# Optimization experiments

Measured on AMD Instinct MI355X. Metric: run time of the kernel, lower is better.

Reference implementation:

```python
import jax, jax.numpy as jnp
import numpy as np

HIDDEN = 512
IN_FEAT = 512


def setup_inputs() -> dict:
    key = jax.random.key(0)
    ks = jax.random.split(key, 6)
    x = jax.random.normal(ks[0], (128, 1024, IN_FEAT), dtype=jnp.float32)
    # LSTM params: concatenated gates in flax order (i, f, g, o)
    s_in = 1.0 / np.sqrt(IN_FEAT)
    s_h = 1.0 / np.sqrt(HIDDEN)
    Wi = jax.random.normal(ks[1], (IN_FEAT, 4 * HIDDEN), dtype=jnp.float32) * s_in
    Wh = jax.random.normal(ks[2], (HIDDEN, 4 * HIDDEN), dtype=jnp.float32) * s_h
    b = jnp.zeros((4 * HIDDEN,), dtype=jnp.float32)
    Wd = jax.random.normal(ks[3], (HIDDEN, 1), dtype=jnp.float32) * s_h
    bd = jnp.zeros((1,), dtype=jnp.float32)
    return {"x": x, "Wi": Wi, "Wh": Wh, "b": b, "Wd": Wd, "bd": bd}


def reference(x, Wi, Wh, b, Wd, bd):
    B, S, _ = x.shape
    H = Wh.shape[0]
    c0 = jnp.zeros((B, H), dtype=x.dtype)
    h0 = jnp.zeros((B, H), dtype=x.dtype)

    def step(carry, xt):
        c, h = carry
        gates = xt @ Wi + h @ Wh + b  # [B, 4H]
        i, f, g, o = jnp.split(gates, 4, axis=-1)
        c_new = jax.nn.sigmoid(f) * c + jax.nn.sigmoid(i) * jnp.tanh(g)
        h_new = jax.nn.sigmoid(o) * jnp.tanh(c_new)
        return (c_new, h_new), None

    (c_T, h_T), _ = jax.lax.scan(step, (c0, h0), jnp.swapaxes(x, 0, 1))
    # Dense(1) on last timestep output, then squeeze
    return (h_T @ Wd + bd).squeeze(-1)
```

## Files before the change

### kernel.cpp

```cpp
#include <hip/hip_runtime.h>

typedef unsigned int u32;
typedef unsigned short u16;
typedef unsigned long long u64;
typedef float f32x4 __attribute__((ext_vector_type(4)));
typedef _Float16 f16x8 __attribute__((ext_vector_type(8)));

#define S_LEN 1024
#define NG 8
#define NM 32
#define GBAT 16
#define PSTR 20

__device__ __forceinline__ u16 f2h_bits(float f) {
  _Float16 h = (_Float16)f;
  return __builtin_bit_cast(u16, h);
}
__device__ __forceinline__ float h2f_bits(u16 b) {
  return (float)__builtin_bit_cast(_Float16, b);
}
__device__ __forceinline__ u32 pk2(float a, float b) {
  return (u32)f2h_bits(a) | ((u32)f2h_bits(b) << 16);
}
__device__ __forceinline__ u32 pkh(u64 v) {
  return (u32)(v & 0xFFFFu) | (((u32)(v >> 32) & 0xFFFFu) << 16);
}

__global__ __launch_bounds__(256) void prep_frags(const float* __restrict__ Wi,
                                                  const float* __restrict__ Wh,
                                                  uint4* __restrict__ wf4) {
  const int blk = blockIdx.x;
  const int m = blk & 31;
  const float* __restrict__ W = (blk & 32) ? Wh : Wi;
  uint4* __restrict__ dst = wf4 + ((blk & 32) ? 131072 : 0) + m * 4096;
  for (int fi = threadIdx.x; fi < 4096; fi += 256) {
    const int lane = fi & 63;
    const int kc = (fi >> 6) & 15;
    const int q = fi >> 10;
    const int gq = lane >> 4, c = lane & 15;
    const int kb = kc * 32 + gq * 8;
    const int gcol = q * 512 + m * 16 + c;
    u32 wds[4];
#pragma unroll
    for (int pp = 0; pp < 4; ++pp) {
      u16 e0 = f2h_bits(W[(size_t)(kb + 2 * pp) * 2048 + gcol]);
      u16 e1 = f2h_bits(W[(size_t)(kb + 2 * pp + 1) * 2048 + gcol]);
      wds[pp] = (u32)e0 | ((u32)e1 << 16);
    }
    uint4 v; v.x = wds[0]; v.y = wds[1]; v.z = wds[2]; v.w = wds[3];
    dst[fi] = v;
  }
}

__global__ __launch_bounds__(256) void lstm_main(
    const float* __restrict__ x,
    const uint4* __restrict__ wif4,
    u32* __restrict__ hbuf,
    const float* __restrict__ bvec,
    const float* __restrict__ Wd,
    const float* __restrict__ bd,
    float* __restrict__ out) {
  __shared__ __align__(16) uint4 sWi[4096];
  __shared__ __align__(16) uint4 sWh[4096];
  __shared__ __align__(16) float pred[16][PSTR * 16];

  const int tid = threadIdx.x;
  const int lane = tid & 63;
  const int wv = tid >> 6;
  const int g = blockIdx.x & 7;
  const int m = blockIdx.x >> 3;

  for (int i = tid; i < 4096; i += 256) {
    sWi[i] = wif4[m * 4096 + i];
    sWh[i] = wif4[131072 + m * 4096 + i];
  }

  const int bt = tid >> 4;
  const int hi_ = tid & 15;
  const int gb = g * GBAT + bt;
  const int hidx = m * 16 + hi_;

  const float bi = bvec[hidx];
  const float bf_ = bvec[512 + hidx];
  const float bg = bvec[1024 + hidx];
  const float bo = bvec[1536 + hidx];
  float c_reg = 0.f;

  const int abt = lane & 15;
  const int oct = lane >> 4;
  const float* __restrict__ xrow = x + (size_t)(g * GBAT + abt) * (S_LEN * 512);
  const u32 hrow_off = ((u32)(g * GBAT + abt)) << 9;

  __syncthreads();

  float4 xa[8], xb[8];
#pragma unroll
  for (int kk = 0; kk < 4; ++kk) {
    const int k0 = ((wv << 2) | kk) * 32 + oct * 8;
    xa[2 * kk]     = *reinterpret_cast<const float4*>(xrow + k0);
    xa[2 * kk + 1] = *reinterpret_cast<const float4*>(xrow + k0 + 4);
  }

  auto step = [&](int t, float4* cur, float4* nxt) {
    {
      int tn = t + 1; tn = (tn < S_LEN) ? tn : (S_LEN - 1);
      const float* xr = xrow + (size_t)tn * 512;
#pragma unroll
      for (int kk = 0; kk < 4; ++kk) {
        const int k0 = ((wv << 2) | kk) * 32 + oct * 8;
        nxt[2 * kk]     = *reinterpret_cast<const float4*>(xr + k0);
        nxt[2 * kk + 1] = *reinterpret_cast<const float4*>(xr + k0 + 4);
      }
    }

    f32x4 acc0 = {0.f, 0.f, 0.f, 0.f}, acc1 = acc0, acc2 = acc0, acc3 = acc0;
#pragma unroll
    for (int kk = 0; kk < 4; ++kk) {
      const int kc = (wv << 2) | kk;
      uint4 av;
      av.x = pk2(cur[2 * kk].x, cur[2 * kk].y);
      av.y = pk2(cur[2 * kk].z, cur[2 * kk].w);
      av.z = pk2(cur[2 * kk + 1].x, cur[2 * kk + 1].y);
      av.w = pk2(cur[2 * kk + 1].z, cur[2 * kk + 1].w);
      f16x8 af = __builtin_bit_cast(f16x8, av);
      acc0 = __builtin_amdgcn_mfma_f32_16x16x32_f16(af, __builtin_bit_cast(f16x8, sWi[(0 * 16 + kc) * 64 + lane]), acc0, 0, 0, 0);
      acc1 = __builtin_amdgcn_mfma_f32_16x16x32_f16(af, __builtin_bit_cast(f16x8, sWi[(1 * 16 + kc) * 64 + lane]), acc1, 0, 0, 0);
      acc2 = __builtin_amdgcn_mfma_f32_16x16x32_f16(af, __builtin_bit_cast(f16x8, sWi[(2 * 16 + kc) * 64 + lane]), acc2, 0, 0, 0);
      acc3 = __builtin_amdgcn_mfma_f32_16x16x32_f16(af, __builtin_bit_cast(f16x8, sWi[(3 * 16 + kc) * 64 + lane]), acc3, 0, 0, 0);
    }

    if (t > 0) {
      const u64* hp = reinterpret_cast<const u64*>(hbuf + (u32)(t & 1) * 65536u + hrow_off);
      const u32 want = (u32)t;
      const u64 wpat = ((u64)want << 16) | ((u64)want << 48);
      u64 raw[4][4];
      for (;;) {
#pragma unroll
        for (int kk = 0; kk < 4; ++kk) {
          const int base = (((wv << 2) | kk) << 4) | (oct << 2);
#pragma unroll
          for (int ee = 0; ee < 4; ++ee)
            raw[kk][ee] = __hip_atomic_load(hp + base + ee, __ATOMIC_RELAXED,
                                            __HIP_MEMORY_SCOPE_AGENT);
        }
        __builtin_amdgcn_sched_barrier(0);
        u64 chk = 0;
#pragma unroll
        for (int kk = 0; kk < 4; ++kk)
#pragma unroll
          for (int ee = 0; ee < 4; ++ee)
            chk |= (raw[kk][ee] ^ wpat) & 0xFFFF0000FFFF0000ull;
        if (__all(chk == 0)) break;
        __builtin_amdgcn_s_sleep(1);
      }
      uint4 hv[4];
#pragma unroll
      for (int kk = 0; kk < 4; ++kk) {
        uint4 t4;
        t4.x = pkh(raw[kk][0]); t4.y = pkh(raw[kk][1]);
        t4.z = pkh(raw[kk][2]); t4.w = pkh(raw[kk][3]);
        hv[kk] = t4;
      }
#pragma unroll
      for (int kk = 0; kk < 4; ++kk) {
        const int kc = (wv << 2) | kk;
        f16x8 hf = __builtin_bit_cast(f16x8, hv[kk]);
        acc0 = __builtin_amdgcn_mfma_f32_16x16x32_f16(hf, __builtin_bit_cast(f16x8, sWh[(0 * 16 + kc) * 64 + lane]), acc0, 0, 0, 0);
        acc1 = __builtin_amdgcn_mfma_f32_16x16x32_f16(hf, __builtin_bit_cast(f16x8, sWh[(1 * 16 + kc) * 64 + lane]), acc1, 0, 0, 0);
        acc2 = __builtin_amdgcn_mfma_f32_16x16x32_f16(hf, __builtin_bit_cast(f16x8, sWh[(2 * 16 + kc) * 64 + lane]), acc2, 0, 0, 0);
        acc3 = __builtin_amdgcn_mfma_f32_16x16x32_f16(hf, __builtin_bit_cast(f16x8, sWh[(3 * 16 + kc) * 64 + lane]), acc3, 0, 0, 0);
      }
    }

    {
      const int cc = lane & 15;
      const int r0 = (lane >> 4) << 2;
      *reinterpret_cast<f32x4*>(&pred[wv * 4 + 0][PSTR * cc + r0]) = acc0;
      *reinterpret_cast<f32x4*>(&pred[wv * 4 + 1][PSTR * cc + r0]) = acc1;
      *reinterpret_cast<f32x4*>(&pred[wv * 4 + 2][PSTR * cc + r0]) = acc2;
      *reinterpret_cast<f32x4*>(&pred[wv * 4 + 3][PSTR * cc + r0]) = acc3;
    }
    asm volatile("s_waitcnt lgkmcnt(0)" ::: "memory");
    __builtin_amdgcn_s_barrier();
    __builtin_amdgcn_sched_barrier(0);

    {
      float gi = bi, gf = bf_, gg = bg, go = bo;
#pragma unroll
      for (int w2 = 0; w2 < 4; ++w2) {
        gi += pred[w2 * 4 + 0][PSTR * hi_ + bt];
        gf += pred[w2 * 4 + 1][PSTR * hi_ + bt];
        gg += pred[w2 * 4 + 2][PSTR * hi_ + bt];
        go += pred[w2 * 4 + 3][PSTR * hi_ + bt];
      }
      const float si = 1.f / (1.f + __expf(-gi));
      const float sf = 1.f / (1.f + __expf(-gf));
      const float so = 1.f / (1.f + __expf(-go));
      c_reg = sf * c_reg + si * tanhf(gg);
      const float hv_ = so * tanhf(c_reg);
      const u32 word = ((u32)(t + 1) << 16) | (u32)f2h_bits(hv_);
      __hip_atomic_store(hbuf + (u32)((t + 1) & 1) * 65536u + (u32)gb * 512u + (u32)hidx,
                         word, __ATOMIC_RELAXED, __HIP_MEMORY_SCOPE_AGENT);
    }
    __builtin_amdgcn_s_barrier();
    __builtin_amdgcn_sched_barrier(0);
  };

  for (int t = 0; t < S_LEN; t += 2) {
    step(t, xa, xb);
    step(t + 1, xb, xa);
  }

  if (m == 0) {
    const int btf = tid >> 4;
    const int part = tid & 15;
    const u64* hp = reinterpret_cast<const u64*>(hbuf + (((u32)(g * GBAT + btf)) << 9));
    const u32 want = (u32)S_LEN;
    const u64 wpat = ((u64)want << 16) | ((u64)want << 48);
    u64 rawv[16];
    for (;;) {
#pragma unroll
      for (int j2 = 0; j2 < 16; ++j2)
        rawv[j2] = __hip_atomic_load(hp + part * 16 + j2, __ATOMIC_RELAXED,
                                     __HIP_MEMORY_SCOPE_AGENT);
      __builtin_amdgcn_sched_barrier(0);
      u64 chk = 0;
#pragma unroll
      for (int j2 = 0; j2 < 16; ++j2)
        chk |= (rawv[j2] ^ wpat) & 0xFFFF0000FFFF0000ull;
      if (__all(chk == 0)) break;
      __builtin_amdgcn_s_sleep(1);
    }
    float acc = 0.f;
#pragma unroll
    for (int j2 = 0; j2 < 16; ++j2) {
      const int k = part * 32 + 2 * j2;
      acc += h2f_bits((u16)(rawv[j2] & 0xFFFFu)) * Wd[k] +
             h2f_bits((u16)((rawv[j2] >> 32) & 0xFFFFu)) * Wd[k + 1];
    }
#pragma unroll
    for (int s = 1; s < 16; s <<= 1) acc += __shfl_xor(acc, s, 64);
    if (part == 0) out[g * GBAT + btf] = acc + bd[0];
  }
}

extern "C" void kernel_launch(void* const* d_in, const int* in_sizes, int n_in,
                              void* d_out, int out_size, void* d_ws, size_t ws_size,
                              hipStream_t stream) {
  const float* x = (const float*)d_in[0];
  const float* Wi = (const float*)d_in[1];
  const float* Wh = (const float*)d_in[2];
  const float* bv = (const float*)d_in[3];
  const float* Wd = (const float*)d_in[4];
  const float* bd = (const float*)d_in[5];
  float* out = (float*)d_out;

  char* ws = (char*)d_ws;
  uint4* wif4 = (uint4*)ws;
  u32* hbuf = (u32*)(ws + (4u << 20));

  hipLaunchKernelGGL(prep_frags, dim3(64), dim3(256), 0, stream, Wi, Wh, wif4);

  const float* kx = x;
  const uint4* kw = wif4;
  u32* kh = hbuf;
  const float* kbv = bv;
  const float* kwd = Wd;
  const float* kbd = bd;
  float* ko = out;
  void* args[] = {&kx, &kw, &kh, &kbv, &kwd, &kbd, &ko};
  hipLaunchCooperativeKernel(reinterpret_cast<void*>(lstm_main), dim3(NG * NM),
                             dim3(256), args, 0, stream);
}
```

Baseline: 4.217 ms.

## Replace per-element tagged h words with per-block step flags and packed fp16 h

Each h value used to carry its own step tag inside a 32-bit word, and consumers polled every word until all tags matched. Producers now write dense packed fp16 pairs, wait for their stores to drain, then one thread per block publishes a step counter. Consumers spin on 32 flags per batch group and then read h once with half the bytes. The next-step x prefetch is moved after the flag wait. The cost is an extra vmcnt(0) wait plus barrier-then-flag latency on the critical path, and correctness now depends on relaxed-ordering visibility between the data stores and the flag store.

```diff
diff --git a/kernel.cpp b/kernel.cpp
--- a/kernel.cpp
+++ b/kernel.cpp
@@ -22,14 +22,13 @@
 __device__ __forceinline__ u32 pk2(float a, float b) {
   return (u32)f2h_bits(a) | ((u32)f2h_bits(b) << 16);
 }
-__device__ __forceinline__ u32 pkh(u64 v) {
-  return (u32)(v & 0xFFFFu) | (((u32)(v >> 32) & 0xFFFFu) << 16);
-}
 
 __global__ __launch_bounds__(256) void prep_frags(const float* __restrict__ Wi,
                                                   const float* __restrict__ Wh,
-                                                  uint4* __restrict__ wf4) {
+                                                  uint4* __restrict__ wf4,
+                                                  u32* __restrict__ flags) {
   const int blk = blockIdx.x;
+  if (blk == 0) flags[threadIdx.x] = 0;
   const int m = blk & 31;
   const float* __restrict__ W = (blk & 32) ? Wh : Wi;
   uint4* __restrict__ dst = wf4 + ((blk & 32) ? 131072 : 0) + m * 4096;
@@ -55,7 +54,8 @@
 __global__ __launch_bounds__(256) void lstm_main(
     const float* __restrict__ x,
     const uint4* __restrict__ wif4,
-    u32* __restrict__ hbuf,
+    u16* __restrict__ hbuf16,
+    u32* __restrict__ flags,
     const float* __restrict__ bvec,
     const float* __restrict__ Wd,
     const float* __restrict__ bd,
@@ -89,7 +89,10 @@
   const int abt = lane & 15;
   const int oct = lane >> 4;
   const float* __restrict__ xrow = x + (size_t)(g * GBAT + abt) * (S_LEN * 512);
-  const u32 hrow_off = ((u32)(g * GBAT + abt)) << 9;
+  const u32 drow = ((u32)(g * GBAT + abt)) * 128u;
+  u32* const hb32 = reinterpret_cast<u32*>(hbuf16);
+  const u64* const hb64 = reinterpret_cast<const u64*>(hbuf16);
+  u32* const flg = flags + g * 32;
 
   __syncthreads();
 
@@ -102,17 +105,6 @@
   }
 
   auto step = [&](int t, float4* cur, float4* nxt) {
-    {
-      int tn = t + 1; tn = (tn < S_LEN) ? tn : (S_LEN - 1);
-      const float* xr = xrow + (size_t)tn * 512;
-#pragma unroll
-      for (int kk = 0; kk < 4; ++kk) {
-        const int k0 = ((wv << 2) | kk) * 32 + oct * 8;
-        nxt[2 * kk]     = *reinterpret_cast<const float4*>(xr + k0);
-        nxt[2 * kk + 1] = *reinterpret_cast<const float4*>(xr + k0 + 4);
-      }
-    }
-
     f32x4 acc0 = {0.f, 0.f, 0.f, 0.f}, acc1 = acc0, acc2 = acc0, acc3 = acc0;
 #pragma unroll
     for (int kk = 0; kk < 4; ++kk) {
@@ -130,45 +122,55 @@
     }
 
     if (t > 0) {
-      const u64* hp = reinterpret_cast<const u64*>(hbuf + (u32)(t & 1) * 65536u + hrow_off);
       const u32 want = (u32)t;
-      const u64 wpat = ((u64)want << 16) | ((u64)want << 48);
-      u64 raw[4][4];
       for (;;) {
+        u32 fv = __hip_atomic_load(flg + (lane & 31), __ATOMIC_RELAXED,
+                                   __HIP_MEMORY_SCOPE_AGENT);
+        if (__all(fv >= want)) break;
+        __builtin_amdgcn_s_sleep(1);
+      }
+      __builtin_amdgcn_sched_barrier(0);
+      asm volatile("" ::: "memory");
+
+      {
+        int tn = t + 1; tn = (tn < S_LEN) ? tn : (S_LEN - 1);
+        const float* xr = xrow + (size_t)tn * 512;
 #pragma unroll
         for (int kk = 0; kk < 4; ++kk) {
-          const int base = (((wv << 2) | kk) << 4) | (oct << 2);
-#pragma unroll
-          for (int ee = 0; ee < 4; ++ee)
-            raw[kk][ee] = __hip_atomic_load(hp + base + ee, __ATOMIC_RELAXED,
-                                            __HIP_MEMORY_SCOPE_AGENT);
+          const int k0 = ((wv << 2) | kk) * 32 + oct * 8;
+          nxt[2 * kk]     = *reinterpret_cast<const float4*>(xr + k0);
+          nxt[2 * kk + 1] = *reinterpret_cast<const float4*>(xr + k0 + 4);
         }
-        __builtin_amdgcn_sched_barrier(0);
-        u64 chk = 0;
-#pragma unroll
-        for (int kk = 0; kk < 4; ++kk)
-#pragma unroll
-          for (int ee = 0; ee < 4; ++ee)
-            chk |= (raw[kk][ee] ^ wpat) & 0xFFFF0000FFFF0000ull;
-        if (__all(chk == 0)) break;
-        __builtin_amdgcn_s_sleep(1);
-      }
-      uint4 hv[4];
+      }
+
+      const u32 dbase = ((u32)(t & 1)) * 16384u + drow;
+      u64 raw[4][2];
 #pragma unroll
       for (int kk = 0; kk < 4; ++kk) {
-        uint4 t4;
-        t4.x = pkh(raw[kk][0]); t4.y = pkh(raw[kk][1]);
-        t4.z = pkh(raw[kk][2]); t4.w = pkh(raw[kk][3]);
-        hv[kk] = t4;
-      }
+        const u32 ci = dbase + (u32)(((wv << 2) | kk) * 8 + oct * 2);
+        raw[kk][0] = __hip_atomic_load(hb64 + ci, __ATOMIC_RELAXED, __HIP_MEMORY_SCOPE_AGENT);
+        raw[kk][1] = __hip_atomic_load(hb64 + ci + 1, __ATOMIC_RELAXED, __HIP_MEMORY_SCOPE_AGENT);
+      }
+      __builtin_amdgcn_sched_barrier(0);
 #pragma unroll
       for (int kk = 0; kk < 4; ++kk) {
         const int kc = (wv << 2) | kk;
-        f16x8 hf = __builtin_bit_cast(f16x8, hv[kk]);
+        uint4 t4;
+        t4.x = (u32)raw[kk][0]; t4.y = (u32)(raw[kk][0] >> 32);
+        t4.z = (u32)raw[kk][1]; t4.w = (u32)(raw[kk][1] >> 32);
+        f16x8 hf = __builtin_bit_cast(f16x8, t4);
         acc0 = __builtin_amdgcn_mfma_f32_16x16x32_f16(hf, __builtin_bit_cast(f16x8, sWh[(0 * 16 + kc) * 64 + lane]), acc0, 0, 0, 0);
         acc1 = __builtin_amdgcn_mfma_f32_16x16x32_f16(hf, __builtin_bit_cast(f16x8, sWh[(1 * 16 + kc) * 64 + lane]), acc1, 0, 0, 0);
         acc2 = __builtin_amdgcn_mfma_f32_16x16x32_f16(hf, __builtin_bit_cast(f16x8, sWh[(2 * 16 + kc) * 64 + lane]), acc2, 0, 0, 0);
         acc3 = __builtin_amdgcn_mfma_f32_16x16x32_f16(hf, __builtin_bit_cast(f16x8, sWh[(3 * 16 + kc) * 64 + lane]), acc3, 0, 0, 0);
+      }
+    } else {
+      const float* xr = xrow + 512;
+#pragma unroll
+      for (int kk = 0; kk < 4; ++kk) {
+        const int k0 = ((wv << 2) | kk) * 32 + oct * 8;
+        nxt[2 * kk]     = *reinterpret_cast<const float4*>(xr + k0);
+        nxt[2 * kk + 1] = *reinterpret_cast<const float4*>(xr + k0 + 4);
       }
     }
 
@@ -198,12 +200,19 @@
       const float so = 1.f / (1.f + __expf(-go));
       c_reg = sf * c_reg + si * tanhf(gg);
       const float hv_ = so * tanhf(c_reg);
-      const u32 word = ((u32)(t + 1) << 16) | (u32)f2h_bits(hv_);
-      __hip_atomic_store(hbuf + (u32)((t + 1) & 1) * 65536u + (u32)gb * 512u + (u32)hidx,
-                         word, __ATOMIC_RELAXED, __HIP_MEMORY_SCOPE_AGENT);
-    }
+      const u32 hb = (u32)f2h_bits(hv_);
+      const u32 partner = __shfl_xor(hb, 1, 64);
+      if ((hi_ & 1) == 0) {
+        const u32 word = hb | (partner << 16);
+        const u32 wi_ = ((u32)((t + 1) & 1)) * 32768u + (u32)gb * 256u + ((u32)hidx >> 1);
+        __hip_atomic_store(hb32 + wi_, word, __ATOMIC_RELAXED, __HIP_MEMORY_SCOPE_AGENT);
+      }
+    }
+    asm volatile("s_waitcnt vmcnt(0)" ::: "memory");
     __builtin_amdgcn_s_barrier();
     __builtin_amdgcn_sched_barrier(0);
+    if (tid == 0)
+      __hip_atomic_store(flg + m, (u32)(t + 1), __ATOMIC_RELAXED, __HIP_MEMORY_SCOPE_AGENT);
   };
 
   for (int t = 0; t < S_LEN; t += 2) {
@@ -214,29 +223,29 @@
   if (m == 0) {
     const int btf = tid >> 4;
     const int part = tid & 15;
-    const u64* hp = reinterpret_cast<const u64*>(hbuf + (((u32)(g * GBAT + btf)) << 9));
-    const u32 want = (u32)S_LEN;
-    const u64 wpat = ((u64)want << 16) | ((u64)want << 48);
-    u64 rawv[16];
     for (;;) {
-#pragma unroll
-      for (int j2 = 0; j2 < 16; ++j2)
-        rawv[j2] = __hip_atomic_load(hp + part * 16 + j2, __ATOMIC_RELAXED,
-                                     __HIP_MEMORY_SCOPE_AGENT);
-      __builtin_amdgcn_sched_barrier(0);
-      u64 chk = 0;
-#pragma unroll
-      for (int j2 = 0; j2 < 16; ++j2)
-        chk |= (rawv[j2] ^ wpat) & 0xFFFF0000FFFF0000ull;
-      if (__all(chk == 0)) break;
+      u32 fv = __hip_atomic_load(flg + (lane & 31), __ATOMIC_RELAXED,
+                                 __HIP_MEMORY_SCOPE_AGENT);
+      if (__all(fv >= (u32)S_LEN)) break;
       __builtin_amdgcn_s_sleep(1);
     }
+    __builtin_amdgcn_sched_barrier(0);
+    asm volatile("" ::: "memory");
+    const u32 rbase = ((u32)(g * GBAT + btf)) * 128u + (u32)part * 8u;
+    u64 rawv[8];
+#pragma unroll
+    for (int j = 0; j < 8; ++j)
+      rawv[j] = __hip_atomic_load(hb64 + rbase + j, __ATOMIC_RELAXED,
+                                  __HIP_MEMORY_SCOPE_AGENT);
+    __builtin_amdgcn_sched_barrier(0);
     float acc = 0.f;
 #pragma unroll
-    for (int j2 = 0; j2 < 16; ++j2) {
-      const int k = part * 32 + 2 * j2;
-      acc += h2f_bits((u16)(rawv[j2] & 0xFFFFu)) * Wd[k] +
-             h2f_bits((u16)((rawv[j2] >> 32) & 0xFFFFu)) * Wd[k + 1];
+    for (int j = 0; j < 8; ++j) {
+      const int k = part * 32 + 4 * j;
+      acc += h2f_bits((u16)(rawv[j] & 0xFFFFu)) * Wd[k] +
+             h2f_bits((u16)((rawv[j] >> 16) & 0xFFFFu)) * Wd[k + 1] +
+             h2f_bits((u16)((rawv[j] >> 32) & 0xFFFFu)) * Wd[k + 2] +
+             h2f_bits((u16)((rawv[j] >> 48) & 0xFFFFu)) * Wd[k + 3];
     }
 #pragma unroll
     for (int s = 1; s < 16; s <<= 1) acc += __shfl_xor(acc, s, 64);
@@ -257,18 +266,20 @@
 
   char* ws = (char*)d_ws;
   uint4* wif4 = (uint4*)ws;
-  u32* hbuf = (u32*)(ws + (4u << 20));
-
-  hipLaunchKernelGGL(prep_frags, dim3(64), dim3(256), 0, stream, Wi, Wh, wif4);
+  u16* hbuf16 = (u16*)(ws + (4u << 20));
+  u32* flags = (u32*)(ws + (4u << 20) + (256u << 10));
+
+  hipLaunchKernelGGL(prep_frags, dim3(64), dim3(256), 0, stream, Wi, Wh, wif4, flags);
 
   const float* kx = x;
   const uint4* kw = wif4;
-  u32* kh = hbuf;
+  u16* kh = hbuf16;
+  u32* kf = flags;
   const float* kbv = bv;
   const float* kwd = Wd;
   const float* kbd = bd;
   float* ko = out;
-  void* args[] = {&kx, &kw, &kh, &kbv, &kwd, &kbd, &ko};
-  hipLaunchCooperativeKernel(reinterpret_cast<void*>(lstm_main), dim3(NG * NM),
-                             dim3(256), args, 0, stream);
-}
+  void* args[] = {&kx, &kw, &kh, &kf, &kbv, &kwd, &kbd, &ko};
+  (void)hipLaunchCooperativeKernel(reinterpret_cast<void*>(lstm_main), dim3(NG * NM),
+                                   dim3(256), args, 0, stream);
+}
```

After: 4.334 ms. 1.03x slower.

## Add XCC-local fast path for h exchange using sc0 vector loads

Applied to the files above, without the earlier changes.

At startup each block records its XCC id and checks whether all 32 blocks of its batch group sit on the same XCC. If they do, the hidden-state exchange polls a second buffer with wide sc0 (cache-coherent within the XCC) dwordx4 loads instead of device-scope atomic loads, and falls back to the atomic path after a bounded spin count. Each h value is written to both buffers. The next-x prefetch is also moved after the h wait to shorten the critical path. This adds redundant stores and depends on how the hardware places blocks, and a missed cross-XCC visibility case could cost up to 512 spins per step before the fallback takes over.

```diff
diff --git a/kernel.cpp b/kernel.cpp
--- a/kernel.cpp
+++ b/kernel.cpp
@@ -5,6 +5,7 @@
 typedef unsigned long long u64;
 typedef float f32x4 __attribute__((ext_vector_type(4)));
 typedef _Float16 f16x8 __attribute__((ext_vector_type(8)));
+typedef u32 u32x4 __attribute__((ext_vector_type(4)));
 
 #define S_LEN 1024
 #define NG 8
@@ -28,8 +29,10 @@
 
 __global__ __launch_bounds__(256) void prep_frags(const float* __restrict__ Wi,
                                                   const float* __restrict__ Wh,
-                                                  uint4* __restrict__ wf4) {
+                                                  uint4* __restrict__ wf4,
+                                                  u32* __restrict__ det) {
   const int blk = blockIdx.x;
+  if (blk == 0) det[threadIdx.x] = 0;
   const int m = blk & 31;
   const float* __restrict__ W = (blk & 32) ? Wh : Wi;
   uint4* __restrict__ dst = wf4 + ((blk & 32) ? 131072 : 0) + m * 4096;
@@ -56,6 +59,8 @@
     const float* __restrict__ x,
     const uint4* __restrict__ wif4,
     u32* __restrict__ hbuf,
+    u32* __restrict__ hbuf2,
+    u32* __restrict__ det,
     const float* __restrict__ bvec,
     const float* __restrict__ Wd,
     const float* __restrict__ bd,
@@ -93,6 +98,24 @@
 
   __syncthreads();
 
+  bool fastw;
+  {
+    u32 myxcc;
+    asm volatile("s_getreg_b32 %0, hwreg(HW_REG_XCC_ID)" : "=s"(myxcc));
+    if (tid == 0)
+      __hip_atomic_store(det + g * 32 + m, myxcc + 1u, __ATOMIC_RELAXED,
+                         __HIP_MEMORY_SCOPE_AGENT);
+    u32 dv;
+    for (;;) {
+      dv = __hip_atomic_load(det + g * 32 + (lane & 31), __ATOMIC_RELAXED,
+                             __HIP_MEMORY_SCOPE_AGENT);
+      if (__all(dv != 0u)) break;
+      __builtin_amdgcn_s_sleep(1);
+    }
+    const u32 d0 = __shfl(dv, 0, 64);
+    fastw = __all(dv == d0);
+  }
+
   float4 xa[8], xb[8];
 #pragma unroll
   for (int kk = 0; kk < 4; ++kk) {
@@ -102,17 +125,6 @@
   }
 
   auto step = [&](int t, float4* cur, float4* nxt) {
-    {
-      int tn = t + 1; tn = (tn < S_LEN) ? tn : (S_LEN - 1);
-      const float* xr = xrow + (size_t)tn * 512;
-#pragma unroll
-      for (int kk = 0; kk < 4; ++kk) {
-        const int k0 = ((wv << 2) | kk) * 32 + oct * 8;
-        nxt[2 * kk]     = *reinterpret_cast<const float4*>(xr + k0);
-        nxt[2 * kk + 1] = *reinterpret_cast<const float4*>(xr + k0 + 4);
-      }
-    }
-
     f32x4 acc0 = {0.f, 0.f, 0.f, 0.f}, acc1 = acc0, acc2 = acc0, acc3 = acc0;
 #pragma unroll
     for (int kk = 0; kk < 4; ++kk) {
@@ -130,37 +142,91 @@
     }
 
     if (t > 0) {
-      const u64* hp = reinterpret_cast<const u64*>(hbuf + (u32)(t & 1) * 65536u + hrow_off);
-      const u32 want = (u32)t;
-      const u64 wpat = ((u64)want << 16) | ((u64)want << 48);
-      u64 raw[4][4];
-      for (;;) {
+      const u32 tg = (u32)t << 16;
+      uint4 hv[4];
+      bool got = false;
+
+      if (fastw) {
+        const u32* p2 = hbuf2 + (((u32)(t & 1)) << 16) + hrow_off +
+                        ((u32)((wv << 7) | (oct << 3)));
+        int spins = 0;
+        for (;;) {
+          u32x4 fA0, fB0, fA1, fB1, fA2, fB2, fA3, fB3;
+          asm volatile("global_load_dwordx4 %0, %1, off sc0" : "=&v"(fA0) : "v"(p2));
+          asm volatile("global_load_dwordx4 %0, %1, off offset:16 sc0" : "=&v"(fB0) : "v"(p2));
+          asm volatile("global_load_dwordx4 %0, %1, off offset:128 sc0" : "=&v"(fA1) : "v"(p2));
+          asm volatile("global_load_dwordx4 %0, %1, off offset:144 sc0" : "=&v"(fB1) : "v"(p2));
+          asm volatile("global_load_dwordx4 %0, %1, off offset:256 sc0" : "=&v"(fA2) : "v"(p2));
+          asm volatile("global_load_dwordx4 %0, %1, off offset:272 sc0" : "=&v"(fB2) : "v"(p2));
+          asm volatile("global_load_dwordx4 %0, %1, off offset:384 sc0" : "=&v"(fA3) : "v"(p2));
+          asm volatile("global_load_dwordx4 %0, %1, off offset:400 sc0" : "=&v"(fB3) : "v"(p2));
+          asm volatile("s_waitcnt vmcnt(0)" ::: "memory");
+          __builtin_amdgcn_sched_barrier(0);
+          u32 bad = (fA0.x ^ tg) | (fA0.y ^ tg) | (fA0.z ^ tg) | (fA0.w ^ tg);
+          bad |= (fB0.x ^ tg) | (fB0.y ^ tg) | (fB0.z ^ tg) | (fB0.w ^ tg);
+          bad |= (fA1.x ^ tg) | (fA1.y ^ tg) | (fA1.z ^ tg) | (fA1.w ^ tg);
+          bad |= (fB1.x ^ tg) | (fB1.y ^ tg) | (fB1.z ^ tg) | (fB1.w ^ tg);
+          bad |= (fA2.x ^ tg) | (fA2.y ^ tg) | (fA2.z ^ tg) | (fA2.w ^ tg);
+          bad |= (fB2.x ^ tg) | (fB2.y ^ tg) | (fB2.z ^ tg) | (fB2.w ^ tg);
+          bad |= (fA3.x ^ tg) | (fA3.y ^ tg) | (fA3.z ^ tg) | (fA3.w ^ tg);
+          bad |= (fB3.x ^ tg) | (fB3.y ^ tg) | (fB3.z ^ tg) | (fB3.w ^ tg);
+          if (__all((bad & 0xFFFF0000u) == 0u)) {
+            hv[0].x = (fA0.x & 0xFFFFu) | (fA0.y << 16); hv[0].y = (fA0.z & 0xFFFFu) | (fA0.w << 16);
+            hv[0].z = (fB0.x & 0xFFFFu) | (fB0.y << 16); hv[0].w = (fB0.z & 0xFFFFu) | (fB0.w << 16);
+            hv[1].x = (fA1.x & 0xFFFFu) | (fA1.y << 16); hv[1].y = (fA1.z & 0xFFFFu) | (fA1.w << 16);
+            hv[1].z = (fB1.x & 0xFFFFu) | (fB1.y << 16); hv[1].w = (fB1.z & 0xFFFFu) | (fB1.w << 16);
+            hv[2].x = (fA2.x & 0xFFFFu) | (fA2.y << 16); hv[2].y = (fA2.z & 0xFFFFu) | (fA2.w << 16);
+            hv[2].z = (fB2.x & 0xFFFFu) | (fB2.y << 16); hv[2].w = (fB2.z & 0xFFFFu) | (fB2.w << 16);
+            hv[3].x = (fA3.x & 0xFFFFu) | (fA3.y << 16); hv[3].y = (fA3.z & 0xFFFFu) | (fA3.w << 16);
+            hv[3].z = (fB3.x & 0xFFFFu) | (fB3.y << 16); hv[3].w = (fB3.z & 0xFFFFu) | (fB3.w << 16);
+            got = true;
+            break;
+          }
+          if (++spins > 512) { fastw = false; break; }
+        }
+      }
+
+      if (!got) {
+        const u64* hp = reinterpret_cast<const u64*>(hbuf + (u32)(t & 1) * 65536u + hrow_off);
+        const u64 wpat = ((u64)tg) | ((u64)tg << 32);
+        u64 raw[4][4];
+        for (;;) {
+#pragma unroll
+          for (int kk = 0; kk < 4; ++kk) {
+            const int base = (((wv << 2) | kk) << 4) | (oct << 2);
+#pragma unroll
+            for (int ee = 0; ee < 4; ++ee)
+              raw[kk][ee] = __hip_atomic_load(hp + base + ee, __ATOMIC_RELAXED,
+                                              __HIP_MEMORY_SCOPE_AGENT);
+          }
+          __builtin_amdgcn_sched_barrier(0);
+          u64 chk = 0;
+#pragma unroll
+          for (int kk = 0; kk < 4; ++kk)
+#pragma unroll
+            for (int ee = 0; ee < 4; ++ee)
+              chk |= (raw[kk][ee] ^ wpat) & 0xFFFF0000FFFF0000ull;
+          if (__all(chk == 0)) break;
+          __builtin_amdgcn_s_sleep(1);
+        }
 #pragma unroll
         for (int kk = 0; kk < 4; ++kk) {
-          const int base = (((wv << 2) | kk) << 4) | (oct << 2);
-#pragma unroll
-          for (int ee = 0; ee < 4; ++ee)
-            raw[kk][ee] = __hip_atomic_load(hp + base + ee, __ATOMIC_RELAXED,
-                                            __HIP_MEMORY_SCOPE_AGENT);
+          hv[kk].x = pkh(raw[kk][0]); hv[kk].y = pkh(raw[kk][1]);
+          hv[kk].z = pkh(raw[kk][2]); hv[kk].w = pkh(raw[kk][3]);
         }
-        __builtin_amdgcn_sched_barrier(0);
-        u64 chk = 0;
-#pragma unroll
-        for (int kk = 0; kk < 4; ++kk)
-#pragma unroll
-          for (int ee = 0; ee < 4; ++ee)
-            chk |= (raw[kk][ee] ^ wpat) & 0xFFFF0000FFFF0000ull;
-        if (__all(chk == 0)) break;
-        __builtin_amdgcn_s_sleep(1);
-      }
-      uint4 hv[4];
-#pragma unroll
-      for (int kk = 0; kk < 4; ++kk) {
-        uint4 t4;
-        t4.x = pkh(raw[kk][0]); t4.y = pkh(raw[kk][1]);
-        t4.z = pkh(raw[kk][2]); t4.w = pkh(raw[kk][3]);
-        hv[kk] = t4;
-      }
+      }
+
+      {
+        int tn = t + 1; tn = (tn < S_LEN) ? tn : (S_LEN - 1);
+        const float* xr = xrow + (size_t)tn * 512;
+#pragma unroll
+        for (int kk = 0; kk < 4; ++kk) {
+          const int k0 = ((wv << 2) | kk) * 32 + oct * 8;
+          nxt[2 * kk]     = *reinterpret_cast<const float4*>(xr + k0);
+          nxt[2 * kk + 1] = *reinterpret_cast<const float4*>(xr + k0 + 4);
+        }
+      }
+
 #pragma unroll
       for (int kk = 0; kk < 4; ++kk) {
         const int kc = (wv << 2) | kk;
@@ -170,6 +236,14 @@
         acc2 = __builtin_amdgcn_mfma_f32_16x16x32_f16(hf, __builtin_bit_cast(f16x8, sWh[(2 * 16 + kc) * 64 + lane]), acc2, 0, 0, 0);
         acc3 = __builtin_amdgcn_mfma_f32_16x16x32_f16(hf, __builtin_bit_cast(f16x8, sWh[(3 * 16 + kc) * 64 + lane]), acc3, 0, 0, 0);
       }
+    } else {
+      const float* xr = xrow + 512;
+#pragma unroll
+      for (int kk = 0; kk < 4; ++kk) {
+        const int k0 = ((wv << 2) | kk) * 32 + oct * 8;
+        nxt[2 * kk]     = *reinterpret_cast<const float4*>(xr + k0);
+        nxt[2 * kk + 1] = *reinterpret_cast<const float4*>(xr + k0 + 4);
+      }
     }
 
     {
@@ -199,8 +273,10 @@
       c_reg = sf * c_reg + si * tanhf(gg);
       const float hv_ = so * tanhf(c_reg);
       const u32 word = ((u32)(t + 1) << 16) | (u32)f2h_bits(hv_);
-      __hip_atomic_store(hbuf + (u32)((t + 1) & 1) * 65536u + (u32)gb * 512u + (u32)hidx,
-                         word, __ATOMIC_RELAXED, __HIP_MEMORY_SCOPE_AGENT);
+      const u32 idx = (u32)((t + 1) & 1) * 65536u + (u32)gb * 512u + (u32)hidx;
+      *reinterpret_cast<volatile u32*>(hbuf2 + idx) = word;
+      __hip_atomic_store(hbuf + idx, word, __ATOMIC_RELAXED,
+                         __HIP_MEMORY_SCOPE_AGENT);
     }
     __builtin_amdgcn_s_barrier();
     __builtin_amdgcn_sched_barrier(0);
@@ -258,17 +334,21 @@
   char* ws = (char*)d_ws;
   uint4* wif4 = (uint4*)ws;
   u32* hbuf = (u32*)(ws + (4u << 20));
-
-  hipLaunchKernelGGL(prep_frags, dim3(64), dim3(256), 0, stream, Wi, Wh, wif4);
+  u32* hbuf2 = (u32*)(ws + (4u << 20) + (512u << 10));
+  u32* det = (u32*)(ws + (5u << 20));
+
+  hipLaunchKernelGGL(prep_frags, dim3(64), dim3(256), 0, stream, Wi, Wh, wif4, det);
 
   const float* kx = x;
   const uint4* kw = wif4;
   u32* kh = hbuf;
+  u32* kh2 = hbuf2;
+  u32* kd = det;
   const float* kbv = bv;
   const float* kwd = Wd;
   const float* kbd = bd;
   float* ko = out;
-  void* args[] = {&kx, &kw, &kh, &kbv, &kwd, &kbd, &ko};
-  hipLaunchCooperativeKernel(reinterpret_cast<void*>(lstm_main), dim3(NG * NM),
-                             dim3(256), args, 0, stream);
-}
+  void* args[] = {&kx, &kw, &kh, &kh2, &kd, &kbv, &kwd, &kbd, &ko};
+  (void)hipLaunchCooperativeKernel(reinterpret_cast<void*>(lstm_main), dim3(NG * NM),
+                                   dim3(256), args, 0, stream);
+}
```

Result: slower. 4.847 ms (+14.9%).
